# Performance work log

Hardware: AMD Instinct MI355X
Metric: run time of the kernel (lower is better)

Reference implementation:

```python
import jax, jax.numpy as jnp
import numpy as np

B, S, D = 4, 2048, 1024
H = 16
DH = D // H

def setup_inputs() -> dict:
    key = jax.random.key(0)
    ks = jax.random.split(key, 5)
    s = 1.0 / np.sqrt(D)
    return {
        "inputs": jax.random.normal(ks[0], (B, S, D), dtype=jnp.float32),
        "Wq": jax.random.normal(ks[1], (D, D), dtype=jnp.float32) * s,
        "Wk": jax.random.normal(ks[2], (D, D), dtype=jnp.float32) * s,
        "Wv": jax.random.normal(ks[3], (D, D), dtype=jnp.float32) * s,
        "Wo": jax.random.normal(ks[4], (D, D), dtype=jnp.float32) * s,
        "bo": jnp.zeros((D,), dtype=jnp.float32),
    }

def reference(inputs, Wq, Wk, Wv, Wo, bo):
    b, s, _ = inputs.shape
    # nn.Linear: y = x @ W.T (no bias for QKV)
    Q = (inputs @ Wq.T).reshape(b, s, H, DH)
    K = (inputs @ Wk.T).reshape(b, s, H, DH)
    V = (inputs @ Wv.T).reshape(b, s, H, DH)
    scores = jnp.einsum("bqhd,bkhd->bhqk", Q, K)  # [B,H,S,S]
    causal = jnp.triu(jnp.ones((s, s), dtype=bool), k=1)
    scores = jnp.where(causal, -jnp.inf, scores)
    w = jax.nn.softmax(scores / np.sqrt(DH), axis=-1)  # dropout p=0.0 -> identity
    Z = jnp.einsum("bhqk,bkhd->bqhd", w, V).reshape(b, s, D)
    return Z @ Wo.T + bo
```

## Files before the change

### kernel.cpp

```cpp
#include <hip/hip_runtime.h>
#include <hip/hip_bf16.h>


#define Bq 4
#define Sq 2048
#define Dq 1024
#define Hq 16
#define DHq 64

typedef __attribute__((ext_vector_type(8))) short short8;
typedef __attribute__((ext_vector_type(4))) float f32x4;
typedef __attribute__((ext_vector_type(2))) unsigned int uint2v;

static __device__ __forceinline__ unsigned short f2bfu(float f) {
    union { __hip_bfloat16 h; unsigned short u; } cv;
    cv.h = __float2bfloat16(f);
    return cv.u;
}
static __device__ __forceinline__ unsigned int cvtpk(float lo, float hi) {
    unsigned int r;
    asm("v_cvt_pk_bf16_f32 %0, %1, %2" : "=v"(r) : "v"(lo), "v"(hi));
    return r;
}

__global__ __launch_bounds__(256) void tobf16(
    const float* __restrict__ X, const float* __restrict__ W0,
    const float* __restrict__ W1, const float* __restrict__ W2,
    const float* __restrict__ W3,
    unsigned short* __restrict__ xb, unsigned short* __restrict__ wb)
{
    const size_t i = ((size_t)blockIdx.x * 256 + threadIdx.x) * 8;
    const size_t NX = (size_t)8388608;
    const float* src; unsigned short* dst; size_t off;
    if (i < NX) { src = X; dst = xb; off = i; }
    else {
        const size_t j = i - NX;
        const int w = (int)(j >> 20);
        off = j & 1048575;
        src = (w == 0) ? W0 : (w == 1) ? W1 : (w == 2) ? W2 : W3;
        dst = wb + ((size_t)w << 20);
    }
    const float4 a = *reinterpret_cast<const float4*>(src + off);
    const float4 b = *reinterpret_cast<const float4*>(src + off + 4);
    short8 v;
    v[0] = (short)f2bfu(a.x); v[1] = (short)f2bfu(a.y);
    v[2] = (short)f2bfu(a.z); v[3] = (short)f2bfu(a.w);
    v[4] = (short)f2bfu(b.x); v[5] = (short)f2bfu(b.y);
    v[6] = (short)f2bfu(b.z); v[7] = (short)f2bfu(b.w);
    *reinterpret_cast<short8*>(dst + off) = v;
}



__global__ __launch_bounds__(256) void mm_qkv(
    const unsigned short* __restrict__ Ab, const unsigned short* __restrict__ Wall,
    unsigned short* __restrict__ oq, unsigned short* __restrict__ ok,
    unsigned short* __restrict__ ovt)
{
    __shared__ unsigned short As[128 * 64];
    __shared__ unsigned short Bs[128 * 64];

    const int z = blockIdx.z;
    const unsigned short* W = Wall + ((size_t)z << 20);

    const int m0 = blockIdx.x * 128, n0 = blockIdx.y * 128;
    const int t = threadIdx.x, lane = t & 63, wave = t >> 6;
    const int g = lane >> 4, c = lane & 15;
    const int wm = wave >> 1, wn = wave & 1;
    const int r8 = lane >> 3, c8 = lane & 7;
    const int ss = (c8 ^ (r8 & 7)) * 8;

    f32x4 acc[4][4] = {};

    for (int kt = 0; kt < 16; ++kt) {
        const int kb = kt * 64;
#pragma unroll
        for (int p = 0; p < 4; ++p) {
            const int rowb = wave * 8 + p * 32;
            const unsigned short* ga = Ab + (size_t)(m0 + rowb + r8) * 1024 + kb + ss;
            const unsigned short* gb = W  + (size_t)(n0 + rowb + r8) * 1024 + kb + ss;
            __builtin_amdgcn_global_load_lds(
                (const __attribute__((address_space(1))) unsigned int*)ga,
                (__attribute__((address_space(3))) unsigned int*)(As + rowb * 64), 16, 0, 0);
            __builtin_amdgcn_global_load_lds(
                (const __attribute__((address_space(1))) unsigned int*)gb,
                (__attribute__((address_space(3))) unsigned int*)(Bs + rowb * 64), 16, 0, 0);
        }
        __syncthreads();
        if (z != 2) {
#pragma unroll
            for (int ks = 0; ks < 2; ++ks) {
                const int sa = ((ks * 4 + g) ^ (c & 7)) * 8;
                short8 bf[4];
#pragma unroll
                for (int nt = 0; nt < 4; ++nt)
                    bf[nt] = *reinterpret_cast<const short8*>(&Bs[(wn * 64 + nt * 16 + c) * 64 + sa]);
#pragma unroll
                for (int mt = 0; mt < 4; ++mt) {
                    const short8 af = *reinterpret_cast<const short8*>(&As[(wm * 64 + mt * 16 + c) * 64 + sa]);
#pragma unroll
                    for (int nt = 0; nt < 4; ++nt)
                        acc[mt][nt] = __builtin_amdgcn_mfma_f32_16x16x32_bf16(af, bf[nt], acc[mt][nt], 0, 0, 0);
                }
            }
        } else {
#pragma unroll
            for (int ks = 0; ks < 2; ++ks) {
                const int sa = ((ks * 4 + g) ^ (c & 7)) * 8;
                short8 bf[4];
#pragma unroll
                for (int nt = 0; nt < 4; ++nt)
                    bf[nt] = *reinterpret_cast<const short8*>(&Bs[(wn * 64 + nt * 16 + c) * 64 + sa]);
#pragma unroll
                for (int mt = 0; mt < 4; ++mt) {
                    const short8 af = *reinterpret_cast<const short8*>(&As[(wm * 64 + mt * 16 + c) * 64 + sa]);
#pragma unroll
                    for (int nt = 0; nt < 4; ++nt)
                        acc[mt][nt] = __builtin_amdgcn_mfma_f32_16x16x32_bf16(bf[nt], af, acc[mt][nt], 0, 0, 0);
                }
            }
        }
        __syncthreads();
    }

    if (z == 2) {
#pragma unroll
        for (int mt = 0; mt < 4; ++mt)
#pragma unroll
            for (int nt = 0; nt < 4; ++nt)
#pragma unroll
                for (int r = 0; r < 4; ++r) {
                    const int m = m0 + wm * 64 + mt * 16 + c;
                    const int n = n0 + wn * 64 + nt * 16 + g * 4 + r;
                    const int bb = m >> 11, s = m & 2047;
                    const int h = n >> 6, d = n & 63;
                    const size_t off = (size_t)(bb * Hq + h) * 131072
                        + (s >> 6) * 4096 + ((d >> 4) & 3) * 1024 + ((s >> 5) & 1) * 512
                        + ((s >> 3) & 3) * 128 + (d & 15) * 8 + (s & 7);
                    ovt[off] = f2bfu(acc[mt][nt][r]);
                }
    } else {
        const float oscale = (z == 0) ? 0.180336880f : 1.0f;
        unsigned short* out = z ? ok : oq;
#pragma unroll
        for (int mt = 0; mt < 4; ++mt)
#pragma unroll
            for (int nt = 0; nt < 4; ++nt)
#pragma unroll
                for (int r = 0; r < 4; ++r) {
                    const int m = m0 + wm * 64 + mt * 16 + g * 4 + r;
                    const int n = n0 + wn * 64 + nt * 16 + c;
                    const int bb = m >> 11, s = m & 2047;
                    const int h = n >> 6, d = n & 63;
                    const size_t off = (size_t)(bb * Hq + h) * 131072
                        + (s >> 4) * 1024 + (d >> 5) * 512 + ((d >> 3) & 3) * 128
                        + (s & 15) * 8 + (d & 7);
                    out[off] = f2bfu(acc[mt][nt][r] * oscale);
                }
    }
}

static __device__ __forceinline__ void stage_kv8(
    const unsigned short* __restrict__ Kb, const unsigned short* __restrict__ Vb,
    int kb, unsigned short* kl, unsigned short* vl, int wave, int lane)
{
    const int off = wave * 512 + lane * 8;
    __builtin_amdgcn_global_load_lds(
        (const __attribute__((address_space(1))) unsigned int*)(Kb + (size_t)kb * 4096 + off),
        (__attribute__((address_space(3))) unsigned int*)(kl + wave * 512), 16, 0, 0);
    __builtin_amdgcn_global_load_lds(
        (const __attribute__((address_space(1))) unsigned int*)(Vb + (size_t)kb * 4096 + off),
        (__attribute__((address_space(3))) unsigned int*)(vl + wave * 512), 16, 0, 0);
}

static __device__ __forceinline__ void pack_p(
    f32x4* st, int rel, int g, int c, unsigned short (*PtW)[72],
    short8& pb0, short8& pb1)
{
    if (rel < 4) {
        const int lim = rel * 16 + c;
#pragma unroll
        for (int kt = 0; kt < 4; ++kt)
#pragma unroll
            for (int r = 0; r < 4; ++r)
                if (kt * 16 + g * 4 + r > lim) st[kt][r] = -3.0e38f;
    }
#pragma unroll
    for (int kt = 0; kt < 4; ++kt) {
        uint2v u;
        u[0] = cvtpk(exp2f(st[kt][0]), exp2f(st[kt][1]));
        u[1] = cvtpk(exp2f(st[kt][2]), exp2f(st[kt][3]));
        *reinterpret_cast<uint2v*>(&PtW[c][kt * 16 + g * 4]) = u;
    }
    pb0 = *reinterpret_cast<const short8*>(&PtW[c][g * 8]);
    pb1 = *reinterpret_cast<const short8*>(&PtW[c][32 + g * 8]);
}

__global__ __launch_bounds__(512, 2) void attn(
    const unsigned short* __restrict__ Qf, const unsigned short* __restrict__ Kf,
    const unsigned short* __restrict__ Vf, unsigned short* __restrict__ O)
{
    __shared__ unsigned short Kl[2][4096];
    __shared__ unsigned short Vl[2][4096];
    __shared__ unsigned short Pt[8][16][72];

    const int bid = blockIdx.x;
    const int half = bid >> 8;
    const int idx = (bid >> 6) & 3;
    const int qq = half ? (3 - idx) : (4 + idx);
    const int bh = (bid & 7) | (((bid >> 3) & 7) << 3);

    const int t = threadIdx.x, lane = t & 63, wave = t >> 6;
    const int g = lane >> 4, c = lane & 15;
    const size_t base = (size_t)bh * (Sq * DHq);
    const unsigned short* Qb = Qf + base;
    const unsigned short* Kb = Kf + base;
    const unsigned short* Vb = Vf + base;
    const int b = bh >> 4, h = bh & 15;

    short8 onesf;
#pragma unroll
    for (int j = 0; j < 8; ++j) onesf[j] = (short)0x3F80;

    const int qtA = qq * 16 + wave * 2;
    const int qtB = qtA + 1;

    const unsigned short* qpA = Qb + (size_t)qtA * 1024 + lane * 8;
    const unsigned short* qpB = Qb + (size_t)qtB * 1024 + lane * 8;
    const short8 qA0 = *reinterpret_cast<const short8*>(qpA);
    const short8 qA1 = *reinterpret_cast<const short8*>(qpA + 512);
    const short8 qB0 = *reinterpret_cast<const short8*>(qpB);
    const short8 qB1 = *reinterpret_cast<const short8*>(qpB + 512);

    f32x4 oA[4] = {}, oB[4] = {};
    f32x4 lA = {}, lB = {};

    const int ibmax = 4 * qq + 3;

    stage_kv8(Kb, Vb, 0, Kl[0], Vl[0], wave, lane);
    __syncthreads();

#pragma unroll 1
    for (int ib = 0; ib <= ibmax; ++ib) {
        const int cur = ib & 1;
        if (ib < ibmax)
            stage_kv8(Kb, Vb, ib + 1, Kl[cur ^ 1], Vl[cur ^ 1], wave, lane);
        __builtin_amdgcn_sched_barrier(0);

        if (4 * ib <= qtA) {
            const unsigned short* kl = &Kl[cur][lane * 8];
            const unsigned short* vl = &Vl[cur][lane * 8];

            f32x4 stA[4] = {}, stB[4] = {};
            __builtin_amdgcn_s_setprio(1);
#pragma unroll
            for (int k2 = 0; k2 < 4; ++k2) {
                const short8 kf0 = *reinterpret_cast<const short8*>(&kl[(2 * k2) * 512]);
                const short8 kf1 = *reinterpret_cast<const short8*>(&kl[(2 * k2 + 1) * 512]);
                stA[k2] = __builtin_amdgcn_mfma_f32_16x16x32_bf16(kf0, qA0, stA[k2], 0, 0, 0);
                stA[k2] = __builtin_amdgcn_mfma_f32_16x16x32_bf16(kf1, qA1, stA[k2], 0, 0, 0);
                stB[k2] = __builtin_amdgcn_mfma_f32_16x16x32_bf16(kf0, qB0, stB[k2], 0, 0, 0);
                stB[k2] = __builtin_amdgcn_mfma_f32_16x16x32_bf16(kf1, qB1, stB[k2], 0, 0, 0);
            }
            __builtin_amdgcn_s_setprio(0);

            short8 pbA0, pbA1, pbB0, pbB1;
            pack_p(stA, qtA - 4 * ib, g, c, Pt[wave], pbA0, pbA1);
            pack_p(stB, qtB - 4 * ib, g, c, Pt[wave], pbB0, pbB1);

            __builtin_amdgcn_s_setprio(1);
            lA = __builtin_amdgcn_mfma_f32_16x16x32_bf16(onesf, pbA0, lA, 0, 0, 0);
            lA = __builtin_amdgcn_mfma_f32_16x16x32_bf16(onesf, pbA1, lA, 0, 0, 0);
            lB = __builtin_amdgcn_mfma_f32_16x16x32_bf16(onesf, pbB0, lB, 0, 0, 0);
            lB = __builtin_amdgcn_mfma_f32_16x16x32_bf16(onesf, pbB1, lB, 0, 0, 0);

#pragma unroll
            for (int dt = 0; dt < 4; ++dt) {
                const short8 vf0 = *reinterpret_cast<const short8*>(&vl[(2 * dt) * 512]);
                const short8 vf1 = *reinterpret_cast<const short8*>(&vl[(2 * dt + 1) * 512]);
                oA[dt] = __builtin_amdgcn_mfma_f32_16x16x32_bf16(vf0, pbA0, oA[dt], 0, 0, 0);
                oA[dt] = __builtin_amdgcn_mfma_f32_16x16x32_bf16(vf1, pbA1, oA[dt], 0, 0, 0);
                oB[dt] = __builtin_amdgcn_mfma_f32_16x16x32_bf16(vf0, pbB0, oB[dt], 0, 0, 0);
                oB[dt] = __builtin_amdgcn_mfma_f32_16x16x32_bf16(vf1, pbB1, oB[dt], 0, 0, 0);
            }
            __builtin_amdgcn_s_setprio(0);
        }
        __syncthreads();
    }

    const float rlA = 1.0f / lA[0];
    const float rlB = 1.0f / lB[0];
    const size_t orowA = ((size_t)b * Sq + qtA * 16 + c) * Dq + h * 64;
    const size_t orowB = ((size_t)b * Sq + qtB * 16 + c) * Dq + h * 64;
#pragma unroll
    for (int dt = 0; dt < 4; ++dt) {
        uint2v uA, uB;
        uA[0] = cvtpk(oA[dt][0] * rlA, oA[dt][1] * rlA);
        uA[1] = cvtpk(oA[dt][2] * rlA, oA[dt][3] * rlA);
        uB[0] = cvtpk(oB[dt][0] * rlB, oB[dt][1] * rlB);
        uB[1] = cvtpk(oB[dt][2] * rlB, oB[dt][3] * rlB);
        *reinterpret_cast<uint2v*>(&O[orowA + dt * 16 + g * 4]) = uA;
        *reinterpret_cast<uint2v*>(&O[orowB + dt * 16 + g * 4]) = uB;
    }
}

__global__ __launch_bounds__(256) void mm_o(
    const unsigned short* __restrict__ Ab, const unsigned short* __restrict__ Wall,
    const float* __restrict__ bo, float* __restrict__ outf)
{
    __shared__ unsigned short As[128 * 64];
    __shared__ unsigned short Bs[128 * 64];

    const unsigned short* W = Wall + ((size_t)3 << 20);

    const int m0 = blockIdx.x * 128, n0 = blockIdx.y * 128;
    const int t = threadIdx.x, lane = t & 63, wave = t >> 6;
    const int g = lane >> 4, c = lane & 15;
    const int wm = wave >> 1, wn = wave & 1;
    const int r8 = lane >> 3, c8 = lane & 7;
    const int ss = (c8 ^ (r8 & 7)) * 8;

    f32x4 acc[4][4] = {};

    for (int kt = 0; kt < 16; ++kt) {
        const int kb = kt * 64;
#pragma unroll
        for (int p = 0; p < 4; ++p) {
            const int rowb = wave * 8 + p * 32;
            const unsigned short* ga = Ab + (size_t)(m0 + rowb + r8) * 1024 + kb + ss;
            const unsigned short* gb = W  + (size_t)(n0 + rowb + r8) * 1024 + kb + ss;
            __builtin_amdgcn_global_load_lds(
                (const __attribute__((address_space(1))) unsigned int*)ga,
                (__attribute__((address_space(3))) unsigned int*)(As + rowb * 64), 16, 0, 0);
            __builtin_amdgcn_global_load_lds(
                (const __attribute__((address_space(1))) unsigned int*)gb,
                (__attribute__((address_space(3))) unsigned int*)(Bs + rowb * 64), 16, 0, 0);
        }
        __syncthreads();
#pragma unroll
        for (int ks = 0; ks < 2; ++ks) {
            const int sa = ((ks * 4 + g) ^ (c & 7)) * 8;
            short8 bf[4];
#pragma unroll
            for (int nt = 0; nt < 4; ++nt)
                bf[nt] = *reinterpret_cast<const short8*>(&Bs[(wn * 64 + nt * 16 + c) * 64 + sa]);
#pragma unroll
            for (int mt = 0; mt < 4; ++mt) {
                const short8 af = *reinterpret_cast<const short8*>(&As[(wm * 64 + mt * 16 + c) * 64 + sa]);
#pragma unroll
                for (int nt = 0; nt < 4; ++nt)
                    acc[mt][nt] = __builtin_amdgcn_mfma_f32_16x16x32_bf16(af, bf[nt], acc[mt][nt], 0, 0, 0);
            }
        }
        __syncthreads();
    }

#pragma unroll
    for (int nt = 0; nt < 4; ++nt) {
        const int n = n0 + wn * 64 + nt * 16 + c;
        const float bias = bo[n];
#pragma unroll
        for (int mt = 0; mt < 4; ++mt)
#pragma unroll
            for (int r = 0; r < 4; ++r) {
                const int m = m0 + wm * 64 + mt * 16 + g * 4 + r;
                outf[(size_t)m * 1024 + n] = acc[mt][nt][r] + bias;
            }
    }
}

extern "C" void kernel_launch(void* const* d_in, const int* in_sizes, int n_in,
                              void* d_out, int out_size, void* d_ws, size_t ws_size,
                              hipStream_t stream) {
    const float* X  = (const float*)d_in[0];
    const float* Wq = (const float*)d_in[1];
    const float* Wk = (const float*)d_in[2];
    const float* Wv = (const float*)d_in[3];
    const float* Wo = (const float*)d_in[4];
    const float* bo = (const float*)d_in[5];
    float* out = (float*)d_out;

    const size_t elems = (size_t)Bq * Hq * Sq * DHq;
    unsigned short* q  = (unsigned short*)d_ws;
    unsigned short* k  = q + elems;
    unsigned short* vt = k + elems;
    unsigned short* xo = vt + elems;
    unsigned short* wb = xo + elems;

    tobf16<<<dim3(6144), 256, 0, stream>>>(X, Wq, Wk, Wv, Wo, xo, wb);

    mm_qkv<<<dim3(64, 8, 3), 256, 0, stream>>>(xo, wb, q, k, vt);

    attn<<<dim3(512), 512, 0, stream>>>(q, k, vt, xo);

    mm_o<<<dim3(64, 8, 1), 256, 0, stream>>>(xo, wb, bo, out);
}
```

Baseline: 183.5 us.

## Pre-swizzle weights into MFMA fragment layout and load B directly from global

The bf16 conversion kernel now writes each weight matrix in a fragment-major layout matching the MFMA 16x16x32 B-operand register order. The QKV and output GEMMs drop the B shared-memory tile and its global-to-LDS copies, and each lane reads its 16-byte B fragment straight from global memory. This removes half of the LDS traffic and staging per K step. In exchange, B loads go through the cache with no LDS sharing between waves, so the two waves with the same wn each fetch that B fragment, and the global load latency is not hidden by prefetch.

Result: slower. 188.1 us (+2.5%).

```diff
diff --git a/kernel.cpp b/kernel.cpp
--- a/kernel.cpp
+++ b/kernel.cpp
@@ -36,9 +36,13 @@
     else {
         const size_t j = i - NX;
         const int w = (int)(j >> 20);
-        off = j & 1048575;
+        const size_t lin = j & 1048575;
         src = (w == 0) ? W0 : (w == 1) ? W1 : (w == 2) ? W2 : W3;
-        dst = wb + ((size_t)w << 20);
+        const int n = (int)(lin >> 10), k0 = (int)(lin & 1023);
+        const size_t foff = (size_t)(n >> 4) * 16384 + (k0 >> 5) * 512
+                          + ((k0 >> 3) & 3) * 128 + (n & 15) * 8;
+        dst = wb + ((size_t)w << 20) + foff - lin;
+        off = lin;
     }
     const float4 a = *reinterpret_cast<const float4*>(src + off);
     const float4 b = *reinterpret_cast<const float4*>(src + off + 4);
@@ -53,15 +57,14 @@
 
 
 __global__ __launch_bounds__(256) void mm_qkv(
-    const unsigned short* __restrict__ Ab, const unsigned short* __restrict__ Wall,
+    const unsigned short* __restrict__ Ab, const unsigned short* __restrict__ Wf,
     unsigned short* __restrict__ oq, unsigned short* __restrict__ ok,
     unsigned short* __restrict__ ovt)
 {
     __shared__ unsigned short As[128 * 64];
-    __shared__ unsigned short Bs[128 * 64];
 
     const int z = blockIdx.z;
-    const unsigned short* W = Wall + ((size_t)z << 20);
+    const unsigned short* Wz = Wf + ((size_t)z << 20);
 
     const int m0 = blockIdx.x * 128, n0 = blockIdx.y * 128;
     const int t = threadIdx.x, lane = t & 63, wave = t >> 6;
@@ -70,6 +73,11 @@
     const int r8 = lane >> 3, c8 = lane & 7;
     const int ss = (c8 ^ (r8 & 7)) * 8;
 
+    const unsigned short* Wtile[4];
+#pragma unroll
+    for (int nt = 0; nt < 4; ++nt)
+        Wtile[nt] = Wz + (size_t)((n0 + wn * 64 + nt * 16) >> 4) * 16384 + lane * 8;
+
     f32x4 acc[4][4] = {};
 
     for (int kt = 0; kt < 16; ++kt) {
@@ -77,14 +85,10 @@
 #pragma unroll
         for (int p = 0; p < 4; ++p) {
             const int rowb = wave * 8 + p * 32;
-            const unsigned short* ga = Ab + (size_t)(m0 + rowb + r8) * 1024 + kb + ss;
-            const unsigned short* gb = W  + (size_t)(n0 + rowb + r8) * 1024 + kb + ss;
             __builtin_amdgcn_global_load_lds(
-                (const __attribute__((address_space(1))) unsigned int*)ga,
+                (const __attribute__((address_space(1))) unsigned int*)(
+                    Ab + (size_t)(m0 + rowb + r8) * 1024 + kb + ss),
                 (__attribute__((address_space(3))) unsigned int*)(As + rowb * 64), 16, 0, 0);
-            __builtin_amdgcn_global_load_lds(
-                (const __attribute__((address_space(1))) unsigned int*)gb,
-                (__attribute__((address_space(3))) unsigned int*)(Bs + rowb * 64), 16, 0, 0);
         }
         __syncthreads();
         if (z != 2) {
@@ -94,7 +98,7 @@
                 short8 bf[4];
 #pragma unroll
                 for (int nt = 0; nt < 4; ++nt)
-                    bf[nt] = *reinterpret_cast<const short8*>(&Bs[(wn * 64 + nt * 16 + c) * 64 + sa]);
+                    bf[nt] = *reinterpret_cast<const short8*>(&Wtile[nt][(kt * 2 + ks) * 512]);
 #pragma unroll
                 for (int mt = 0; mt < 4; ++mt) {
                     const short8 af = *reinterpret_cast<const short8*>(&As[(wm * 64 + mt * 16 + c) * 64 + sa]);
@@ -110,7 +114,7 @@
                 short8 bf[4];
 #pragma unroll
                 for (int nt = 0; nt < 4; ++nt)
-                    bf[nt] = *reinterpret_cast<const short8*>(&Bs[(wn * 64 + nt * 16 + c) * 64 + sa]);
+                    bf[nt] = *reinterpret_cast<const short8*>(&Wtile[nt][(kt * 2 + ks) * 512]);
 #pragma unroll
                 for (int mt = 0; mt < 4; ++mt) {
                     const short8 af = *reinterpret_cast<const short8*>(&As[(wm * 64 + mt * 16 + c) * 64 + sa]);
@@ -305,13 +309,12 @@
 }
 
 __global__ __launch_bounds__(256) void mm_o(
-    const unsigned short* __restrict__ Ab, const unsigned short* __restrict__ Wall,
+    const unsigned short* __restrict__ Ab, const unsigned short* __restrict__ Wf,
     const float* __restrict__ bo, float* __restrict__ outf)
 {
     __shared__ unsigned short As[128 * 64];
-    __shared__ unsigned short Bs[128 * 64];
-
-    const unsigned short* W = Wall + ((size_t)3 << 20);
+
+    const unsigned short* Wz = Wf + ((size_t)3 << 20);
 
     const int m0 = blockIdx.x * 128, n0 = blockIdx.y * 128;
     const int t = threadIdx.x, lane = t & 63, wave = t >> 6;
@@ -320,6 +323,11 @@
     const int r8 = lane >> 3, c8 = lane & 7;
     const int ss = (c8 ^ (r8 & 7)) * 8;
 
+    const unsigned short* Wtile[4];
+#pragma unroll
+    for (int nt = 0; nt < 4; ++nt)
+        Wtile[nt] = Wz + (size_t)((n0 + wn * 64 + nt * 16) >> 4) * 16384 + lane * 8;
+
     f32x4 acc[4][4] = {};
 
     for (int kt = 0; kt < 16; ++kt) {
@@ -327,14 +335,10 @@
 #pragma unroll
         for (int p = 0; p < 4; ++p) {
             const int rowb = wave * 8 + p * 32;
-            const unsigned short* ga = Ab + (size_t)(m0 + rowb + r8) * 1024 + kb + ss;
-            const unsigned short* gb = W  + (size_t)(n0 + rowb + r8) * 1024 + kb + ss;
             __builtin_amdgcn_global_load_lds(
-                (const __attribute__((address_space(1))) unsigned int*)ga,
+                (const __attribute__((address_space(1))) unsigned int*)(
+                    Ab + (size_t)(m0 + rowb + r8) * 1024 + kb + ss),
                 (__attribute__((address_space(3))) unsigned int*)(As + rowb * 64), 16, 0, 0);
-            __builtin_amdgcn_global_load_lds(
-                (const __attribute__((address_space(1))) unsigned int*)gb,
-                (__attribute__((address_space(3))) unsigned int*)(Bs + rowb * 64), 16, 0, 0);
         }
         __syncthreads();
 #pragma unroll
@@ -343,7 +347,7 @@
             short8 bf[4];
 #pragma unroll
             for (int nt = 0; nt < 4; ++nt)
-                bf[nt] = *reinterpret_cast<const short8*>(&Bs[(wn * 64 + nt * 16 + c) * 64 + sa]);
+                bf[nt] = *reinterpret_cast<const short8*>(&Wtile[nt][(kt * 2 + ks) * 512]);
 #pragma unroll
             for (int mt = 0; mt < 4; ++mt) {
                 const short8 af = *reinterpret_cast<const short8*>(&As[(wm * 64 + mt * 16 + c) * 64 + sa]);
```

## Double-buffer LDS tiles in QKV and output projection GEMMs

Applied to the files above, without the earlier changes.

Both projection GEMM kernels now keep two LDS buffers per operand. Each iteration issues the global-to-LDS loads for the next K-tile before running the MFMA work on the current tile, replacing the old load-barrier-compute sequence. The goal is to hide global load latency behind matrix math inside a single block. In exchange, LDS per block doubles to 64KB, which can lower the number of resident blocks per CU and the latency hiding that came from running several blocks at once.

After: 183.5 us. About the same (+0.0%).

```diff
diff --git a/kernel.cpp b/kernel.cpp
--- a/kernel.cpp
+++ b/kernel.cpp
@@ -57,8 +57,8 @@
     unsigned short* __restrict__ oq, unsigned short* __restrict__ ok,
     unsigned short* __restrict__ ovt)
 {
-    __shared__ unsigned short As[128 * 64];
-    __shared__ unsigned short Bs[128 * 64];
+    __shared__ unsigned short As[2][128 * 64];
+    __shared__ unsigned short Bs[2][128 * 64];
 
     const int z = blockIdx.z;
     const unsigned short* W = Wall + ((size_t)z << 20);
@@ -72,21 +72,31 @@
 
     f32x4 acc[4][4] = {};
 
+#define STAGE_QKV(KT, BUF)                                                      \
+    {                                                                           \
+        const int kb_ = (KT) * 64;                                              \
+        _Pragma("unroll")                                                       \
+        for (int p = 0; p < 4; ++p) {                                           \
+            const int rowb = wave * 8 + p * 32;                                 \
+            __builtin_amdgcn_global_load_lds(                                   \
+                (const __attribute__((address_space(1))) unsigned int*)(        \
+                    Ab + (size_t)(m0 + rowb + r8) * 1024 + kb_ + ss),           \
+                (__attribute__((address_space(3))) unsigned int*)(&As[BUF][rowb * 64]), 16, 0, 0); \
+            __builtin_amdgcn_global_load_lds(                                   \
+                (const __attribute__((address_space(1))) unsigned int*)(        \
+                    W + (size_t)(n0 + rowb + r8) * 1024 + kb_ + ss),            \
+                (__attribute__((address_space(3))) unsigned int*)(&Bs[BUF][rowb * 64]), 16, 0, 0); \
+        }                                                                       \
+    }
+
+    STAGE_QKV(0, 0);
+    __syncthreads();
+
+#pragma unroll 1
     for (int kt = 0; kt < 16; ++kt) {
-        const int kb = kt * 64;
-#pragma unroll
-        for (int p = 0; p < 4; ++p) {
-            const int rowb = wave * 8 + p * 32;
-            const unsigned short* ga = Ab + (size_t)(m0 + rowb + r8) * 1024 + kb + ss;
-            const unsigned short* gb = W  + (size_t)(n0 + rowb + r8) * 1024 + kb + ss;
-            __builtin_amdgcn_global_load_lds(
-                (const __attribute__((address_space(1))) unsigned int*)ga,
-                (__attribute__((address_space(3))) unsigned int*)(As + rowb * 64), 16, 0, 0);
-            __builtin_amdgcn_global_load_lds(
-                (const __attribute__((address_space(1))) unsigned int*)gb,
-                (__attribute__((address_space(3))) unsigned int*)(Bs + rowb * 64), 16, 0, 0);
-        }
-        __syncthreads();
+        const int cur = kt & 1;
+        if (kt < 15) STAGE_QKV(kt + 1, cur ^ 1);
+
         if (z != 2) {
 #pragma unroll
             for (int ks = 0; ks < 2; ++ks) {
@@ -94,10 +104,10 @@
                 short8 bf[4];
 #pragma unroll
                 for (int nt = 0; nt < 4; ++nt)
-                    bf[nt] = *reinterpret_cast<const short8*>(&Bs[(wn * 64 + nt * 16 + c) * 64 + sa]);
+                    bf[nt] = *reinterpret_cast<const short8*>(&Bs[cur][(wn * 64 + nt * 16 + c) * 64 + sa]);
 #pragma unroll
                 for (int mt = 0; mt < 4; ++mt) {
-                    const short8 af = *reinterpret_cast<const short8*>(&As[(wm * 64 + mt * 16 + c) * 64 + sa]);
+                    const short8 af = *reinterpret_cast<const short8*>(&As[cur][(wm * 64 + mt * 16 + c) * 64 + sa]);
 #pragma unroll
                     for (int nt = 0; nt < 4; ++nt)
                         acc[mt][nt] = __builtin_amdgcn_mfma_f32_16x16x32_bf16(af, bf[nt], acc[mt][nt], 0, 0, 0);
@@ -110,10 +120,10 @@
                 short8 bf[4];
 #pragma unroll
                 for (int nt = 0; nt < 4; ++nt)
-                    bf[nt] = *reinterpret_cast<const short8*>(&Bs[(wn * 64 + nt * 16 + c) * 64 + sa]);
+                    bf[nt] = *reinterpret_cast<const short8*>(&Bs[cur][(wn * 64 + nt * 16 + c) * 64 + sa]);
 #pragma unroll
                 for (int mt = 0; mt < 4; ++mt) {
-                    const short8 af = *reinterpret_cast<const short8*>(&As[(wm * 64 + mt * 16 + c) * 64 + sa]);
+                    const short8 af = *reinterpret_cast<const short8*>(&As[cur][(wm * 64 + mt * 16 + c) * 64 + sa]);
 #pragma unroll
                     for (int nt = 0; nt < 4; ++nt)
                         acc[mt][nt] = __builtin_amdgcn_mfma_f32_16x16x32_bf16(bf[nt], af, acc[mt][nt], 0, 0, 0);
@@ -122,6 +132,7 @@
         }
         __syncthreads();
     }
+#undef STAGE_QKV
 
     if (z == 2) {
 #pragma unroll
@@ -308,8 +319,8 @@
     const unsigned short* __restrict__ Ab, const unsigned short* __restrict__ Wall,
     const float* __restrict__ bo, float* __restrict__ outf)
 {
-    __shared__ unsigned short As[128 * 64];
-    __shared__ unsigned short Bs[128 * 64];
+    __shared__ unsigned short As[2][128 * 64];
+    __shared__ unsigned short Bs[2][128 * 64];
 
     const unsigned short* W = Wall + ((size_t)3 << 20);
 
@@ -322,31 +333,41 @@
 
     f32x4 acc[4][4] = {};
 
+#define STAGE_O(KT, BUF)                                                        \
+    {                                                                           \
+        const int kb_ = (KT) * 64;                                              \
+        _Pragma("unroll")                                                       \
+        for (int p = 0; p < 4; ++p) {                                           \
+            const int rowb = wave * 8 + p * 32;                                 \
+            __builtin_amdgcn_global_load_lds(                                   \
+                (const __attribute__((address_space(1))) unsigned int*)(        \
+                    Ab + (size_t)(m0 + rowb + r8) * 1024 + kb_ + ss),           \
+                (__attribute__((address_space(3))) unsigned int*)(&As[BUF][rowb * 64]), 16, 0, 0); \
+            __builtin_amdgcn_global_load_lds(                                   \
+                (const __attribute__((address_space(1))) unsigned int*)(        \
+                    W + (size_t)(n0 + rowb + r8) * 1024 + kb_ + ss),            \
+                (__attribute__((address_space(3))) unsigned int*)(&Bs[BUF][rowb * 64]), 16, 0, 0); \
+        }                                                                       \
+    }
+
+    STAGE_O(0, 0);
+    __syncthreads();
+
+#pragma unroll 1
     for (int kt = 0; kt < 16; ++kt) {
-        const int kb = kt * 64;
-#pragma unroll
-        for (int p = 0; p < 4; ++p) {
-            const int rowb = wave * 8 + p * 32;
-            const unsigned short* ga = Ab + (size_t)(m0 + rowb + r8) * 1024 + kb + ss;
-            const unsigned short* gb = W  + (size_t)(n0 + rowb + r8) * 1024 + kb + ss;
-            __builtin_amdgcn_global_load_lds(
-                (const __attribute__((address_space(1))) unsigned int*)ga,
-                (__attribute__((address_space(3))) unsigned int*)(As + rowb * 64), 16, 0, 0);
-            __builtin_amdgcn_global_load_lds(
-                (const __attribute__((address_space(1))) unsigned int*)gb,
-                (__attribute__((address_space(3))) unsigned int*)(Bs + rowb * 64), 16, 0, 0);
-        }
-        __syncthreads();
+        const int cur = kt & 1;
+        if (kt < 15) STAGE_O(kt + 1, cur ^ 1);
+
 #pragma unroll
         for (int ks = 0; ks < 2; ++ks) {
             const int sa = ((ks * 4 + g) ^ (c & 7)) * 8;
             short8 bf[4];
 #pragma unroll
             for (int nt = 0; nt < 4; ++nt)
-                bf[nt] = *reinterpret_cast<const short8*>(&Bs[(wn * 64 + nt * 16 + c) * 64 + sa]);
+                bf[nt] = *reinterpret_cast<const short8*>(&Bs[cur][(wn * 64 + nt * 16 + c) * 64 + sa]);
 #pragma unroll
             for (int mt = 0; mt < 4; ++mt) {
-                const short8 af = *reinterpret_cast<const short8*>(&As[(wm * 64 + mt * 16 + c) * 64 + sa]);
+                const short8 af = *reinterpret_cast<const short8*>(&As[cur][(wm * 64 + mt * 16 + c) * 64 + sa]);
 #pragma unroll
                 for (int nt = 0; nt < 4; ++nt)
                     acc[mt][nt] = __builtin_amdgcn_mfma_f32_16x16x32_bf16(af, bf[nt], acc[mt][nt], 0, 0, 0);
@@ -354,6 +375,7 @@
         }
         __syncthreads();
     }
+#undef STAGE_O
 
 #pragma unroll
     for (int nt = 0; nt < 4; ++nt) {
```
